# Kernel tuning notes

Hardware: AMD Instinct MI355X
Metric: run time of the kernel (lower is better)

Reference implementation:

```python
import jax, jax.numpy as jnp
import numpy as np

D_MODEL = 1024
T = 4096

def setup_inputs() -> dict:
    key = jax.random.key(0)
    k1, k2, k3 = jax.random.split(key, 3)
    x = jax.random.normal(k1, (T, D_MODEL), dtype=jnp.float32)
    # original uses torch.rand (uniform [0,1)) for params
    Wqk = jax.random.uniform(k2, (D_MODEL, D_MODEL), dtype=jnp.float32)
    Wov = jax.random.uniform(k3, (D_MODEL, D_MODEL), dtype=jnp.float32)
    return {"x": x, "Wqk": Wqk, "Wov": Wov}

def reference(x, Wqk, Wov):
    Tcur = x.shape[0]
    # scores = softmax(x @ Wqk @ x^T + causal_mask)
    q = x @ Wqk                              # [T, d]
    logits = q @ x.T                         # [T, T]
    causal = jnp.tril(jnp.ones((Tcur, Tcur), dtype=bool))
    logits = jnp.where(causal, logits, -jnp.inf)
    attn = jax.nn.softmax(logits, axis=-1)   # [T, T]
    out = (attn @ x) @ Wov                   # [T, d]
    return out
```

## Files before the change

kernel.cpp:

```cpp
#include <hip/hip_runtime.h>
#include <hip/hip_fp16.h>

#define T_DIM 4096
#define D_DIM 1024

typedef _Float16 f16;
typedef _Float16 f16x4 __attribute__((ext_vector_type(4)));
typedef _Float16 f16x8 __attribute__((ext_vector_type(8)));
typedef float f32x4 __attribute__((ext_vector_type(4)));

#define GAS __attribute__((address_space(1)))
#define LAS __attribute__((address_space(3)))

__global__ void split4(const float* __restrict__ in, f16* __restrict__ hi,
                       f16* __restrict__ lo) {
    int i = (blockIdx.x * 256 + threadIdx.x) * 4;
    float4 v = *(const float4*)(in + i);
    float vv[4] = {v.x, v.y, v.z, v.w};
    f16x4 h, l;
#pragma unroll
    for (int j = 0; j < 4; ++j) {
        f16 hh = (f16)vv[j];
        h[j] = hh;
        l[j] = (f16)(vv[j] - (float)hh);
    }
    *(f16x4*)(hi + i) = h;
    *(f16x4*)(lo + i) = l;
}

__global__ void transpose_split(const float* __restrict__ in, f16* __restrict__ hi,
                                f16* __restrict__ lo, int R, int C) {
    __shared__ float t[32][33];
    int tx = threadIdx.x & 31;
    int ty = threadIdx.x >> 5;
#pragma unroll
    for (int q = 0; q < 4; ++q) {
        int r = blockIdx.y * 32 + ty + q * 8;
        int c = blockIdx.x * 32 + tx;
        t[ty + q * 8][tx] = in[(size_t)r * C + c];
    }
    __syncthreads();
#pragma unroll
    for (int q = 0; q < 4; ++q) {
        int c = blockIdx.x * 32 + ty + q * 8;
        int r = blockIdx.y * 32 + tx;
        float v = t[tx][ty + q * 8];
        size_t idx = (size_t)c * R + r;
        f16 h = (f16)v;
        hi[idx] = h;
        lo[idx] = (f16)(v - (float)h);
    }
}

__device__ __forceinline__ void stage128x32(const f16* __restrict__ src, int ld,
                                            f16* lds_tile, int w, int l) {
#pragma unroll
    for (int q = 0; q < 2; ++q) {
        int p = (w * 2 + q) * 64 + l;
        int r = p >> 2;
        int c = (p & 3) ^ ((r >> 1) & 3);
        const f16* g = src + r * ld + c * 8;
        f16* d = lds_tile + (w * 2 + q) * 512;
        __builtin_amdgcn_global_load_lds((const GAS void*)g, (LAS void*)d, 16, 0, 0);
    }
}

template <bool SPLIT3, int OUT_MODE, bool CAUSAL_SKIP, bool KCAP_CAUSAL>
__global__ __launch_bounds__(256) void gemm_nt(
    const f16* __restrict__ Ah, const f16* __restrict__ Al,
    const f16* __restrict__ Bh, const f16* __restrict__ Bl,
    float* __restrict__ Cf, f16* __restrict__ Ch, f16* __restrict__ Cl,
    int M, int N, int K) {
    const int row0 = blockIdx.y * 128;
    const int col0 = blockIdx.x * 128;
    if (CAUSAL_SKIP) {
        if (col0 > row0 + 127) return;
    }
    int Keff = K;
    if (KCAP_CAUSAL) {
        Keff = row0 + 128;
        if (Keff > K) Keff = K;
    }

    constexpr int NT = SPLIT3 ? 4 : 2;
    constexpr int TILE = 128 * 32;
    __shared__ f16 lds[2 * NT * TILE];

    const int tid = threadIdx.x;
    const int w = tid >> 6, l = tid & 63;
    const int wm = w >> 1, wn = w & 1;
    const int lr = l & 15;
    const int kg = l >> 4;
    const int cswz = kg ^ ((lr >> 1) & 3);
    const int aoff = (wm * 64 + lr) * 32 + cswz * 8;
    const int boff = (wn * 64 + lr) * 32 + cswz * 8;

    const f16* Asrc = Ah + (size_t)row0 * K;
    const f16* Bsrc = Bh + (size_t)col0 * K;
    const f16* Asrc_l = SPLIT3 ? Al + (size_t)row0 * K : nullptr;
    const f16* Bsrc_l = SPLIT3 ? Bl + (size_t)col0 * K : nullptr;

    auto stage_all = [&](int buf, int k0) {
        f16* base = lds + buf * NT * TILE;
        stage128x32(Asrc + k0, K, base + 0 * TILE, w, l);
        stage128x32(Bsrc + k0, K, base + 1 * TILE, w, l);
        if constexpr (SPLIT3) {
            stage128x32(Asrc_l + k0, K, base + 2 * TILE, w, l);
            stage128x32(Bsrc_l + k0, K, base + 3 * TILE, w, l);
        }
    };

    f32x4 acc[4][4] = {};

    stage_all(0, 0);
    __syncthreads();

    int cur = 0;
    for (int k0 = 0; k0 < Keff; k0 += 32) {
        const f16* base = lds + cur * NT * TILE;
        const f16* Ah_t = base;
        const f16* Bh_t = base + 1 * TILE;
        const f16* Al_t = base + 2 * TILE;
        const f16* Bl_t = base + 3 * TILE;

        f16x8 ah[4], bh[4], al[4], bl[4];
#pragma unroll
        for (int m = 0; m < 4; ++m) {
            ah[m] = *(const f16x8*)&Ah_t[aoff + m * 512];
            if constexpr (SPLIT3) al[m] = *(const f16x8*)&Al_t[aoff + m * 512];
        }
#pragma unroll
        for (int n = 0; n < 4; ++n) {
            bh[n] = *(const f16x8*)&Bh_t[boff + n * 512];
            if constexpr (SPLIT3) bl[n] = *(const f16x8*)&Bl_t[boff + n * 512];
        }

        const int kn = k0 + 32;
        if (kn < Keff) stage_all(cur ^ 1, kn);

#pragma unroll
        for (int m = 0; m < 4; ++m)
#pragma unroll
            for (int n = 0; n < 4; ++n) {
                acc[m][n] = __builtin_amdgcn_mfma_f32_16x16x32_f16(ah[m], bh[n],
                                                                   acc[m][n], 0, 0, 0);
                if constexpr (SPLIT3) {
                    acc[m][n] = __builtin_amdgcn_mfma_f32_16x16x32_f16(
                        al[m], bh[n], acc[m][n], 0, 0, 0);
                    acc[m][n] = __builtin_amdgcn_mfma_f32_16x16x32_f16(
                        ah[m], bl[n], acc[m][n], 0, 0, 0);
                }
            }

        __syncthreads();
        cur ^= 1;
    }

#pragma unroll
    for (int m = 0; m < 4; ++m)
#pragma unroll
        for (int n = 0; n < 4; ++n)
#pragma unroll
            for (int j = 0; j < 4; ++j) {
                int row = row0 + wm * 64 + m * 16 + kg * 4 + j;
                int col = col0 + wn * 64 + n * 16 + lr;
                size_t idx = (size_t)row * N + col;
                float v = acc[m][n][j];
                if constexpr (OUT_MODE == 0) {
                    Cf[idx] = v;
                } else if constexpr (OUT_MODE == 1) {
                    f16 h = (f16)v;
                    Ch[idx] = h;
                    Cl[idx] = (f16)(v - (float)h);
                } else {
                    Ch[idx] = (f16)v;
                }
            }
}

__global__ void softmax_causal(const float* __restrict__ L, f16* __restrict__ A) {
    const int i = blockIdx.x;
    const int n = i + 1;
    const int tid = threadIdx.x;
    const float* row = L + (size_t)i * T_DIM;
    f16* arow = A + (size_t)i * T_DIM;

    float m = -INFINITY, s = 0.f;
    for (int j = tid; j < n; j += 256) {
        float v = row[j];
        if (v > m) {
            s = s * __expf(m - v) + 1.f;
            m = v;
        } else {
            s += __expf(v - m);
        }
    }

    __shared__ float sm[256], ss[256];
    sm[tid] = m;
    ss[tid] = s;
    __syncthreads();
    for (int o = 128; o > 0; o >>= 1) {
        if (tid < o) {
            float m1 = sm[tid], s1 = ss[tid];
            float m2 = sm[tid + o], s2 = ss[tid + o];
            float M = fmaxf(m1, m2);
            float S = (M == -INFINITY) ? 0.f
                                       : s1 * __expf(m1 - M) + s2 * __expf(m2 - M);
            sm[tid] = M;
            ss[tid] = S;
        }
        __syncthreads();
    }
    const float M = sm[0];
    const float inv = 1.f / ss[0];

    const int jmax = ((i >> 7) + 1) << 7;
    for (int j = tid; j < jmax; j += 256) {
        float v = (j < n) ? __expf(row[j] - M) * inv : 0.f;
        arow[j] = (f16)v;
    }
}

extern "C" void kernel_launch(void* const* d_in, const int* in_sizes, int n_in,
                              void* d_out, int out_size, void* d_ws, size_t ws_size,
                              hipStream_t stream) {
    (void)in_sizes; (void)n_in; (void)out_size; (void)ws_size;
    const float* x = (const float*)d_in[0];
    const float* wqk = (const float*)d_in[1];
    const float* wov = (const float*)d_in[2];
    float* out = (float*)d_out;
    char* ws = (char*)d_ws;
    const size_t MB = 1024 * 1024;

    f16* x_hi    = (f16*)(ws + 0 * MB);
    f16* x_lo    = (f16*)(ws + 8 * MB);
    f16* wqkT_hi = (f16*)(ws + 16 * MB);
    f16* wqkT_lo = (f16*)(ws + 18 * MB);
    f16* wovT_hi = (f16*)(ws + 20 * MB);
    f16* wovT_lo = (f16*)(ws + 22 * MB);
    f16* xT_hi   = (f16*)(ws + 24 * MB);
    f16* xT_lo   = (f16*)(ws + 32 * MB);
    f16* q_hi    = (f16*)(ws + 40 * MB);
    f16* q_lo    = (f16*)(ws + 48 * MB);
    f16* z_hi    = (f16*)(ws + 56 * MB);
    f16* attn    = (f16*)(ws + 64 * MB);
    float* logit = (float*)(ws + 96 * MB);

    split4<<<(T_DIM * D_DIM) / 1024, 256, 0, stream>>>(x, x_hi, x_lo);
    transpose_split<<<dim3(D_DIM / 32, D_DIM / 32), 256, 0, stream>>>(
        wqk, wqkT_hi, wqkT_lo, D_DIM, D_DIM);
    transpose_split<<<dim3(D_DIM / 32, D_DIM / 32), 256, 0, stream>>>(
        wov, wovT_hi, wovT_lo, D_DIM, D_DIM);
    transpose_split<<<dim3(D_DIM / 32, T_DIM / 32), 256, 0, stream>>>(
        x, xT_hi, xT_lo, T_DIM, D_DIM);

    gemm_nt<true, 1, false, false>
        <<<dim3(D_DIM / 128, T_DIM / 128), 256, 0, stream>>>(
            x_hi, x_lo, wqkT_hi, wqkT_lo, nullptr, q_hi, q_lo, T_DIM, D_DIM, D_DIM);

    gemm_nt<true, 0, true, false>
        <<<dim3(T_DIM / 128, T_DIM / 128), 256, 0, stream>>>(
            q_hi, q_lo, x_hi, x_lo, logit, nullptr, nullptr, T_DIM, T_DIM, D_DIM);

    softmax_causal<<<T_DIM, 256, 0, stream>>>(logit, attn);

    gemm_nt<false, 2, false, true>
        <<<dim3(D_DIM / 128, T_DIM / 128), 256, 0, stream>>>(
            attn, nullptr, xT_hi, nullptr, nullptr, z_hi, nullptr, T_DIM, D_DIM, T_DIM);

    gemm_nt<false, 0, false, false>
        <<<dim3(D_DIM / 128, T_DIM / 128), 256, 0, stream>>>(
            z_hi, nullptr, wovT_hi, nullptr, out, nullptr, nullptr, T_DIM, D_DIM, D_DIM);
}
```

Before: 315.6 us.

## Template GEMM tile shape, use 128x64 tiles, reverse causal row order

Parameterizes the GEMM kernel on tile M/N sizes and switches the three 1024-wide-output GEMMs to 128x64 tiles, doubling their block counts to 512 to better fill the GPU's compute units. Adds a reversed row order for the causal attn@x GEMM so the longest (largest-K) row blocks are scheduled first, reducing tail imbalance. It also moves the next-tile prefetch before the LDS fragment reads. Smaller tiles lower per-block data reuse and raise global/LDS traffic per flop.

```diff
diff --git a/kernel.cpp b/kernel.cpp
--- a/kernel.cpp
+++ b/kernel.cpp
@@ -52,39 +52,46 @@
     }
 }
 
-__device__ __forceinline__ void stage128x32(const f16* __restrict__ src, int ld,
-                                            f16* lds_tile, int w, int l) {
-#pragma unroll
-    for (int q = 0; q < 2; ++q) {
-        int p = (w * 2 + q) * 64 + l;
+template <int ROWS>
+__device__ __forceinline__ void stage_tile(const f16* __restrict__ src, int ld,
+                                           f16* lds_tile, int w, int l) {
+    constexpr int ITER = (ROWS * 4) / 256;
+#pragma unroll
+    for (int q = 0; q < ITER; ++q) {
+        int p = q * 256 + w * 64 + l;
         int r = p >> 2;
         int c = (p & 3) ^ ((r >> 1) & 3);
         const f16* g = src + r * ld + c * 8;
-        f16* d = lds_tile + (w * 2 + q) * 512;
+        f16* d = lds_tile + (q * 256 + w * 64) * 8;
         __builtin_amdgcn_global_load_lds((const GAS void*)g, (LAS void*)d, 16, 0, 0);
     }
 }
 
-template <bool SPLIT3, int OUT_MODE, bool CAUSAL_SKIP, bool KCAP_CAUSAL>
+template <int TM, int TN, bool SPLIT3, int OUT_MODE, bool CAUSAL_SKIP,
+          bool KCAP_CAUSAL, bool REVY>
 __global__ __launch_bounds__(256) void gemm_nt(
     const f16* __restrict__ Ah, const f16* __restrict__ Al,
     const f16* __restrict__ Bh, const f16* __restrict__ Bl,
     float* __restrict__ Cf, f16* __restrict__ Ch, f16* __restrict__ Cl,
     int M, int N, int K) {
-    const int row0 = blockIdx.y * 128;
-    const int col0 = blockIdx.x * 128;
+    const int by = REVY ? (gridDim.y - 1 - blockIdx.y) : blockIdx.y;
+    const int row0 = by * TM;
+    const int col0 = blockIdx.x * TN;
     if (CAUSAL_SKIP) {
-        if (col0 > row0 + 127) return;
+        if (col0 > row0 + TM - 1) return;
     }
     int Keff = K;
     if (KCAP_CAUSAL) {
-        Keff = row0 + 128;
+        Keff = row0 + TM;
         if (Keff > K) Keff = K;
     }
 
-    constexpr int NT = SPLIT3 ? 4 : 2;
-    constexpr int TILE = 128 * 32;
-    __shared__ f16 lds[2 * NT * TILE];
+    constexpr int TILE_A = TM * 32;
+    constexpr int TILE_B = TN * 32;
+    constexpr int BUFSZ = (SPLIT3 ? 2 : 1) * (TILE_A + TILE_B);
+    constexpr int M_REP = TM / 32;
+    constexpr int N_REP = TN / 32;
+    __shared__ f16 lds[2 * BUFSZ];
 
     const int tid = threadIdx.x;
     const int w = tid >> 6, l = tid & 63;
@@ -92,8 +99,8 @@
     const int lr = l & 15;
     const int kg = l >> 4;
     const int cswz = kg ^ ((lr >> 1) & 3);
-    const int aoff = (wm * 64 + lr) * 32 + cswz * 8;
-    const int boff = (wn * 64 + lr) * 32 + cswz * 8;
+    const int aoff = (wm * (TM / 2) + lr) * 32 + cswz * 8;
+    const int boff = (wn * (TN / 2) + lr) * 32 + cswz * 8;
 
     const f16* Asrc = Ah + (size_t)row0 * K;
     const f16* Bsrc = Bh + (size_t)col0 * K;
@@ -101,47 +108,47 @@
     const f16* Bsrc_l = SPLIT3 ? Bl + (size_t)col0 * K : nullptr;
 
     auto stage_all = [&](int buf, int k0) {
-        f16* base = lds + buf * NT * TILE;
-        stage128x32(Asrc + k0, K, base + 0 * TILE, w, l);
-        stage128x32(Bsrc + k0, K, base + 1 * TILE, w, l);
+        f16* base = lds + buf * BUFSZ;
+        stage_tile<TM>(Asrc + k0, K, base, w, l);
+        stage_tile<TN>(Bsrc + k0, K, base + TILE_A, w, l);
         if constexpr (SPLIT3) {
-            stage128x32(Asrc_l + k0, K, base + 2 * TILE, w, l);
-            stage128x32(Bsrc_l + k0, K, base + 3 * TILE, w, l);
+            stage_tile<TM>(Asrc_l + k0, K, base + TILE_A + TILE_B, w, l);
+            stage_tile<TN>(Bsrc_l + k0, K, base + 2 * TILE_A + TILE_B, w, l);
         }
     };
 
-    f32x4 acc[4][4] = {};
+    f32x4 acc[M_REP][N_REP] = {};
 
     stage_all(0, 0);
     __syncthreads();
 
     int cur = 0;
     for (int k0 = 0; k0 < Keff; k0 += 32) {
-        const f16* base = lds + cur * NT * TILE;
+        const int kn = k0 + 32;
+        if (kn < Keff) stage_all(cur ^ 1, kn);
+
+        const f16* base = lds + cur * BUFSZ;
         const f16* Ah_t = base;
-        const f16* Bh_t = base + 1 * TILE;
-        const f16* Al_t = base + 2 * TILE;
-        const f16* Bl_t = base + 3 * TILE;
-
-        f16x8 ah[4], bh[4], al[4], bl[4];
-#pragma unroll
-        for (int m = 0; m < 4; ++m) {
+        const f16* Bh_t = base + TILE_A;
+        const f16* Al_t = base + TILE_A + TILE_B;
+        const f16* Bl_t = base + 2 * TILE_A + TILE_B;
+
+        f16x8 ah[M_REP], bh[N_REP], al[M_REP], bl[N_REP];
+#pragma unroll
+        for (int m = 0; m < M_REP; ++m) {
             ah[m] = *(const f16x8*)&Ah_t[aoff + m * 512];
             if constexpr (SPLIT3) al[m] = *(const f16x8*)&Al_t[aoff + m * 512];
         }
 #pragma unroll
-        for (int n = 0; n < 4; ++n) {
+        for (int n = 0; n < N_REP; ++n) {
             bh[n] = *(const f16x8*)&Bh_t[boff + n * 512];
             if constexpr (SPLIT3) bl[n] = *(const f16x8*)&Bl_t[boff + n * 512];
         }
 
-        const int kn = k0 + 32;
-        if (kn < Keff) stage_all(cur ^ 1, kn);
-
-#pragma unroll
-        for (int m = 0; m < 4; ++m)
-#pragma unroll
-            for (int n = 0; n < 4; ++n) {
+#pragma unroll
+        for (int m = 0; m < M_REP; ++m)
+#pragma unroll
+            for (int n = 0; n < N_REP; ++n) {
                 acc[m][n] = __builtin_amdgcn_mfma_f32_16x16x32_f16(ah[m], bh[n],
                                                                    acc[m][n], 0, 0, 0);
                 if constexpr (SPLIT3) {
@@ -157,13 +164,13 @@
     }
 
 #pragma unroll
-    for (int m = 0; m < 4; ++m)
-#pragma unroll
-        for (int n = 0; n < 4; ++n)
+    for (int m = 0; m < M_REP; ++m)
+#pragma unroll
+        for (int n = 0; n < N_REP; ++n)
 #pragma unroll
             for (int j = 0; j < 4; ++j) {
-                int row = row0 + wm * 64 + m * 16 + kg * 4 + j;
-                int col = col0 + wn * 64 + n * 16 + lr;
+                int row = row0 + wm * (TM / 2) + m * 16 + kg * 4 + j;
+                int col = col0 + wn * (TN / 2) + n * 16 + lr;
                 size_t idx = (size_t)row * N + col;
                 float v = acc[m][n][j];
                 if constexpr (OUT_MODE == 0) {
@@ -255,21 +262,21 @@
     transpose_split<<<dim3(D_DIM / 32, T_DIM / 32), 256, 0, stream>>>(
         x, xT_hi, xT_lo, T_DIM, D_DIM);
 
-    gemm_nt<true, 1, false, false>
-        <<<dim3(D_DIM / 128, T_DIM / 128), 256, 0, stream>>>(
+    gemm_nt<128, 64, true, 1, false, false, false>
+        <<<dim3(D_DIM / 64, T_DIM / 128), 256, 0, stream>>>(
             x_hi, x_lo, wqkT_hi, wqkT_lo, nullptr, q_hi, q_lo, T_DIM, D_DIM, D_DIM);
 
-    gemm_nt<true, 0, true, false>
+    gemm_nt<128, 128, true, 0, true, false, false>
         <<<dim3(T_DIM / 128, T_DIM / 128), 256, 0, stream>>>(
             q_hi, q_lo, x_hi, x_lo, logit, nullptr, nullptr, T_DIM, T_DIM, D_DIM);
 
     softmax_causal<<<T_DIM, 256, 0, stream>>>(logit, attn);
 
-    gemm_nt<false, 2, false, true>
-        <<<dim3(D_DIM / 128, T_DIM / 128), 256, 0, stream>>>(
+    gemm_nt<128, 64, false, 2, false, true, true>
+        <<<dim3(D_DIM / 64, T_DIM / 128), 256, 0, stream>>>(
             attn, nullptr, xT_hi, nullptr, nullptr, z_hi, nullptr, T_DIM, D_DIM, T_DIM);
 
-    gemm_nt<false, 0, false, false>
-        <<<dim3(D_DIM / 128, T_DIM / 128), 256, 0, stream>>>(
+    gemm_nt<128, 64, false, 0, false, false, false>
+        <<<dim3(D_DIM / 64, T_DIM / 128), 256, 0, stream>>>(
             z_hi, nullptr, wovT_hi, nullptr, out, nullptr, nullptr, T_DIM, D_DIM, D_DIM);
 }
```

Measured after the change: 291.9 us. 1.08x faster.
